# Kernel tuning notes

Hardware: AMD Instinct MI355X
Metric: run time of the kernel (lower is better)

## Reference

```python
import jax, jax.numpy as jnp
import numpy as np

EPS_NORM = 1e-12  # torch F.normalize eps
EPS_PI = 1e-8


def _l2_normalize(x, axis):
    n = jnp.sqrt(jnp.sum(x * x, axis=axis, keepdims=True))
    return x / jnp.maximum(n, EPS_NORM)


def setup_inputs() -> dict:
    key = jax.random.key(0)
    k1, _ = jax.random.split(key)
    B, L, H, E = 8, 1024, 8, 64
    queries = jax.random.normal(k1, (B, L, H, E), dtype=jnp.float32)
    temp = jnp.ones((H, 1), dtype=jnp.float32)  # nn.Parameter(torch.ones(num_heads, 1))
    return {"queries": queries, "temp": temp}


def reference(queries, temp):
    # queries: [B, L, H, E] -> w: [B, H, N, d]
    w = jnp.transpose(queries, (0, 2, 1, 3))
    # normalize over token dim (-2), square, sum over feature dim -> energy [B,H,N]
    w_normed = _l2_normalize(w, axis=-2)
    energy = jnp.sum(w_normed * w_normed, axis=-1)
    # softmax over the HEAD dim (nn.Softmax(dim=1)); temp [H,1] broadcasts over N
    Pi = jax.nn.softmax(energy * temp[None, :, :], axis=1)  # [B,H,N]
    # cosine-similarity attention matrix, mapped to [0,1]
    w_unit = _l2_normalize(w, axis=-1)
    attn_matrix = (jnp.einsum('bhnd,bhmd->bhnm', w_unit, w_unit) + 1.0) * 0.5
    # Pi normalized over tokens
    Pi_norm = Pi / (jnp.sum(Pi, axis=-1, keepdims=True) + EPS_PI)
    # dots: [B,H,1,d] = Pi_norm^T (w**2)
    dots = jnp.einsum('bhn,bhnd->bhd', Pi_norm, w * w)[:, :, None, :]
    attn = 1.0 / (1.0 + dots)  # [B,H,1,d]
    out = -(w * Pi[..., None]) * attn  # [B,H,N,d]
    out = jnp.transpose(out, (0, 2, 1, 3))  # [B,L,H,E]
    attn_reshaped = jnp.transpose(attn_matrix, (0, 2, 1, 3))  # [B,N,H,N]
    return out, attn_reshaped
```

## Files before the change

### kernel.cpp

```cpp
#include <hip/hip_runtime.h>
#include <hip/hip_bf16.h>

#define B_ 8
#define N_ 1024
#define H_ 8
#define D_ 64

typedef __attribute__((ext_vector_type(8))) short short8;
typedef __attribute__((ext_vector_type(4))) float f32x4;

__global__ __launch_bounds__(256) void k_zero(float* __restrict__ p, int n) {
    const int i = blockIdx.x * 256 + threadIdx.x;
    if (i < n) p[i] = 0.f;
}

__global__ __launch_bounds__(256) void k_colsum(const float* __restrict__ q,
                                                ushort* __restrict__ wunit,
                                                float* __restrict__ colsum) {
    const int bh = blockIdx.x, chunk = blockIdx.y;
    const int b = bh >> 3, h = bh & 7;
    const float* qb = q + (size_t)(b * N_ * H_ + h) * D_;
    __shared__ float red[16][64];
    const int t = threadIdx.x;
    const int ng = t >> 4;
    const int dq = (t & 15) * 4;
    float cx = 0.f, cy = 0.f, cz = 0.f, cw = 0.f;
    #pragma unroll
    for (int i = 0; i < 8; ++i) {
        const int n = chunk * 128 + ng + i * 16;
        const float4 v = *(const float4*)(qb + (size_t)n * (H_ * D_) + dq);
        cx += v.x * v.x; cy += v.y * v.y; cz += v.z * v.z; cw += v.w * v.w;
        float ss = v.x * v.x + v.y * v.y + v.z * v.z + v.w * v.w;
        ss += __shfl_xor(ss, 1, 16);
        ss += __shfl_xor(ss, 2, 16);
        ss += __shfl_xor(ss, 4, 16);
        ss += __shfl_xor(ss, 8, 16);
        const float invr = 1.0f / fmaxf(sqrtf(ss), 1e-12f);
        __hip_bfloat162 p0 =
            __float22bfloat162_rn(make_float2(v.x * invr, v.y * invr));
        __hip_bfloat162 p1 =
            __float22bfloat162_rn(make_float2(v.z * invr, v.w * invr));
        uint2 pk;
        pk.x = *(unsigned int*)&p0;
        pk.y = *(unsigned int*)&p1;
        *(uint2*)(wunit + ((size_t)bh * N_ + n) * D_ + dq) = pk;
    }
    red[ng][dq + 0] = cx; red[ng][dq + 1] = cy;
    red[ng][dq + 2] = cz; red[ng][dq + 3] = cw;
    __syncthreads();
    if (t < 64) {
        float s = 0.f;
        #pragma unroll
        for (int i = 0; i < 16; ++i) s += red[i][t];
        atomicAdd(&colsum[bh * 64 + t], s);
    }
}

__global__ __launch_bounds__(256) void k_energy(const float* __restrict__ q,
                                                const float* __restrict__ colsum,
                                                float* __restrict__ energy) {
    const int bh = blockIdx.x, chunk = blockIdx.y;
    const int b = bh >> 3, h = bh & 7;
    __shared__ float inv2[64];
    const int t = threadIdx.x;
    if (t < 64) inv2[t] = 1.0f / fmaxf(colsum[bh * 64 + t], 1e-24f);
    __syncthreads();
    const int n = chunk * 256 + t;
    const float4* row =
        (const float4*)(q + (size_t)(b * N_ * H_ + h) * D_ + (size_t)n * (H_ * D_));
    float e = 0.f;
    #pragma unroll
    for (int i = 0; i < 16; ++i) {
        const float4 v = row[i];
        e += v.x * v.x * inv2[4 * i + 0] + v.y * v.y * inv2[4 * i + 1] +
             v.z * v.z * inv2[4 * i + 2] + v.w * v.w * inv2[4 * i + 3];
    }
    energy[(size_t)bh * N_ + n] = e;
}

__global__ __launch_bounds__(256) void k_pi(const float* __restrict__ energy,
                                            const float* __restrict__ temp,
                                            float* __restrict__ Pi,
                                            float* __restrict__ Pisum) {
    const int idx = blockIdx.x * 256 + threadIdx.x;
    const int b = idx >> 10, n = idx & (N_ - 1);
    float e[H_];
    float m = -1e30f;
    #pragma unroll
    for (int h = 0; h < H_; ++h) {
        e[h] = energy[(size_t)(b * H_ + h) * N_ + n] * temp[h];
        m = fmaxf(m, e[h]);
    }
    float s = 0.f;
    #pragma unroll
    for (int h = 0; h < H_; ++h) { e[h] = expf(e[h] - m); s += e[h]; }
    const float inv = 1.0f / s;
    #pragma unroll
    for (int h = 0; h < H_; ++h) {
        const float p = e[h] * inv;
        Pi[(size_t)(b * H_ + h) * N_ + n] = p;
        float w = p;
        #pragma unroll
        for (int off = 32; off; off >>= 1) w += __shfl_xor(w, off, 64);
        if ((threadIdx.x & 63) == 0) atomicAdd(&Pisum[b * H_ + h], w);
    }
}

__global__ __launch_bounds__(256) void k_dots(const float* __restrict__ q,
                                              const float* __restrict__ Pi,
                                              float* __restrict__ dots) {
    const int bh = blockIdx.x, chunk = blockIdx.y;
    const int b = bh >> 3, h = bh & 7;
    const float* qb = q + (size_t)(b * N_ * H_ + h) * D_;
    const float* Pib = Pi + (size_t)bh * N_;
    __shared__ float red[16][64];
    const int t = threadIdx.x, ng = t >> 4, dq = (t & 15) * 4;
    float cx = 0.f, cy = 0.f, cz = 0.f, cw = 0.f;
    #pragma unroll
    for (int i = 0; i < 8; ++i) {
        const int n = chunk * 128 + ng + i * 16;
        const float p = Pib[n];
        const float4 v = *(const float4*)(qb + (size_t)n * (H_ * D_) + dq);
        cx += p * v.x * v.x; cy += p * v.y * v.y;
        cz += p * v.z * v.z; cw += p * v.w * v.w;
    }
    red[ng][dq + 0] = cx; red[ng][dq + 1] = cy;
    red[ng][dq + 2] = cz; red[ng][dq + 3] = cw;
    __syncthreads();
    if (t < 64) {
        float s = 0.f;
        #pragma unroll
        for (int i = 0; i < 16; ++i) s += red[i][t];
        atomicAdd(&dots[bh * 64 + t], s);
    }
}

__global__ __launch_bounds__(256) void k_attn(const float* __restrict__ dots,
                                              const float* __restrict__ Pisum,
                                              float* __restrict__ attnv) {
    const int i = blockIdx.x * 256 + threadIdx.x;
    const int bh = i >> 6;
    const float invS = 1.0f / (Pisum[bh] + 1e-8f);
    attnv[i] = 1.0f / (1.0f + dots[i] * invS);
}

__global__ __launch_bounds__(256) void k_outw(const float* __restrict__ q,
                                              const float* __restrict__ Pi,
                                              const float* __restrict__ attnv,
                                              float* __restrict__ out0) {
    const int bh = blockIdx.x, chunk = blockIdx.y;
    const int b = bh >> 3, h = bh & 7;
    __shared__ float av[64];
    const int t = threadIdx.x;
    if (t < 64) av[t] = attnv[bh * 64 + t];
    __syncthreads();
    const int n = chunk * 256 + t;
    const float p = -Pi[(size_t)bh * N_ + n];
    const float4* row =
        (const float4*)(q + (size_t)(b * N_ * H_ + h) * D_ + (size_t)n * (H_ * D_));
    float4* orow = (float4*)(out0 + ((size_t)(b * N_ + n) * H_ + h) * D_);
    #pragma unroll
    for (int i = 0; i < 16; ++i) {
        const float4 v = row[i];
        orow[i] = make_float4(v.x * p * av[4 * i + 0], v.y * p * av[4 * i + 1],
                              v.z * p * av[4 * i + 2], v.w * p * av[4 * i + 3]);
    }
}

__global__ __launch_bounds__(256) void k_gram(const ushort* __restrict__ wunit,
                                              float* __restrict__ out1) {
    const int bh = blockIdx.y;
    const int b = bh >> 3, h = bh & 7;
    const int tn = blockIdx.x & 7, tm = blockIdx.x >> 3;
    __shared__ __align__(16) char smem[36864];
    ushort(*lA)[72] = (ushort(*)[72])smem;
    ushort(*lB)[72] = (ushort(*)[72])(smem + 18432);
    float* stg = (float*)smem;
    const int t = threadIdx.x;
    const ushort* Ub = wunit + (size_t)bh * N_ * D_;

    {
        const uint4* gA = (const uint4*)(Ub + (size_t)tn * 128 * D_);
        const uint4* gB = (const uint4*)(Ub + (size_t)tm * 128 * D_);
        #pragma unroll
        for (int c = 0; c < 4; ++c) {
            const int idx = t + c * 256;
            const int row = idx >> 3, col8 = (idx & 7) * 8;
            *(uint4*)&lA[row][col8] = gA[idx];
            *(uint4*)&lB[row][col8] = gB[idx];
        }
    }
    __syncthreads();

    const int wave = t >> 6, lane = t & 63;
    const int rbase = wave * 32;
    const int arow = lane & 15;
    const int kq = (lane >> 4) * 8;

    f32x4 acc[2][8];
    #pragma unroll
    for (int i = 0; i < 2; ++i)
        #pragma unroll
        for (int j = 0; j < 8; ++j) acc[i][j] = (f32x4){0.f, 0.f, 0.f, 0.f};

    #pragma unroll
    for (int kk = 0; kk < 2; ++kk) {
        const int ko = kk * 32 + kq;
        const short8 a0 = *(const short8*)&lA[rbase + arow][ko];
        const short8 a1 = *(const short8*)&lA[rbase + 16 + arow][ko];
        #pragma unroll
        for (int tc = 0; tc < 8; ++tc) {
            const short8 bfr = *(const short8*)&lB[tc * 16 + arow][ko];
            acc[0][tc] = __builtin_amdgcn_mfma_f32_16x16x32_bf16(
                a0, bfr, acc[0][tc], 0, 0, 0);
            acc[1][tc] = __builtin_amdgcn_mfma_f32_16x16x32_bf16(
                a1, bfr, acc[1][tc], 0, 0, 0);
        }
    }
    __syncthreads();

    float* ms = stg + wave * 2112;
    const int col = lane & 15, rq = (lane >> 4) * 4;
    #pragma unroll
    for (int tr = 0; tr < 2; ++tr) {
        #pragma unroll
        for (int tc = 0; tc < 8; ++tc)
            #pragma unroll
            for (int r = 0; r < 4; ++r)
                ms[(rq + r) * 132 + tc * 16 + col] =
                    (acc[tr][tc][r] + 1.0f) * 0.5f;
        #pragma unroll
        for (int i = 0; i < 8; ++i) {
            const int f = i * 64 + lane;
            const int r2 = f >> 5, c2 = f & 31;
            const float4 v = *(const float4*)&ms[r2 * 132 + c2 * 4];
            const int n = tn * 128 + wave * 32 + tr * 16 + r2;
            const int m = tm * 128 + c2 * 4;
            *(float4*)&out1[((size_t)(b * N_ + n) * H_ + h) * N_ + m] = v;
        }
    }
}

extern "C" void kernel_launch(void* const* d_in, const int* in_sizes, int n_in,
                              void* d_out, int out_size, void* d_ws,
                              size_t ws_size, hipStream_t stream) {
    const float* q = (const float*)d_in[0];
    const float* temp = (const float*)d_in[1];
    float* out0 = (float*)d_out;
    float* out1 = out0 + (size_t)B_ * N_ * H_ * D_;

    char* ws = (char*)d_ws;
    ushort* wunit = (ushort*)ws;
    float* Pi     = (float*)(ws + 8388608);
    float* energy = (float*)(ws + 8650752);
    float* colsum = (float*)(ws + 8912896);
    float* dots   = (float*)(ws + 8929280);
    float* Pisum  = (float*)(ws + 8945664);
    float* attnv  = (float*)(ws + 8945920);

    k_zero<<<33, 256, 0, stream>>>(colsum, 8256);
    k_colsum<<<dim3(64, 8), 256, 0, stream>>>(q, wunit, colsum);
    k_energy<<<dim3(64, 4), 256, 0, stream>>>(q, colsum, energy);
    k_pi<<<32, 256, 0, stream>>>(energy, temp, Pi, Pisum);
    k_dots<<<dim3(64, 8), 256, 0, stream>>>(q, Pi, dots);
    k_attn<<<16, 256, 0, stream>>>(dots, Pisum, attnv);
    k_outw<<<dim3(64, 4), 256, 0, stream>>>(q, Pi, attnv, out0);
    k_gram<<<dim3(64, 64), 256, 0, stream>>>(wunit, out1);
}
```

Measured before the change: 334.2 us.

## Fuse reduction kernels per head and restructure Gram kernel with LDS swizzle

After: 347.1 us. +3.8%, slower.

```diff
diff --git a/kernel.cpp b/kernel.cpp
--- a/kernel.cpp
+++ b/kernel.cpp
@@ -9,25 +9,26 @@
 typedef __attribute__((ext_vector_type(8))) short short8;
 typedef __attribute__((ext_vector_type(4))) float f32x4;
 
-__global__ __launch_bounds__(256) void k_zero(float* __restrict__ p, int n) {
-    const int i = blockIdx.x * 256 + threadIdx.x;
-    if (i < n) p[i] = 0.f;
-}
-
-__global__ __launch_bounds__(256) void k_colsum(const float* __restrict__ q,
-                                                ushort* __restrict__ wunit,
-                                                float* __restrict__ colsum) {
-    const int bh = blockIdx.x, chunk = blockIdx.y;
+#define GLL(g, l)                                                         \
+    __builtin_amdgcn_global_load_lds(                                     \
+        (const __attribute__((address_space(1))) unsigned int*)(g),       \
+        (__attribute__((address_space(3))) unsigned int*)(l), 16, 0, 0)
+
+__global__ __launch_bounds__(1024) void k_prep(const float* __restrict__ q,
+                                               ushort* __restrict__ wunit,
+                                               float* __restrict__ energy) {
+    const int bh = blockIdx.x;
     const int b = bh >> 3, h = bh & 7;
     const float* qb = q + (size_t)(b * N_ * H_ + h) * D_;
-    __shared__ float red[16][64];
+    __shared__ float red[64][68];
+    __shared__ float inv2[64];
     const int t = threadIdx.x;
     const int ng = t >> 4;
     const int dq = (t & 15) * 4;
     float cx = 0.f, cy = 0.f, cz = 0.f, cw = 0.f;
     #pragma unroll
-    for (int i = 0; i < 8; ++i) {
-        const int n = chunk * 128 + ng + i * 16;
+    for (int i = 0; i < 16; ++i) {
+        const int n = i * 64 + ng;
         const float4 v = *(const float4*)(qb + (size_t)n * (H_ * D_) + dq);
         cx += v.x * v.x; cy += v.y * v.y; cz += v.z * v.z; cw += v.w * v.w;
         float ss = v.x * v.x + v.y * v.y + v.z * v.z + v.w * v.w;
@@ -45,29 +46,16 @@
         pk.y = *(unsigned int*)&p1;
         *(uint2*)(wunit + ((size_t)bh * N_ + n) * D_ + dq) = pk;
     }
-    red[ng][dq + 0] = cx; red[ng][dq + 1] = cy;
-    red[ng][dq + 2] = cz; red[ng][dq + 3] = cw;
+    *(float4*)&red[ng][dq] = make_float4(cx, cy, cz, cw);
     __syncthreads();
     if (t < 64) {
         float s = 0.f;
         #pragma unroll
-        for (int i = 0; i < 16; ++i) s += red[i][t];
-        atomicAdd(&colsum[bh * 64 + t], s);
-    }
-}
-
-__global__ __launch_bounds__(256) void k_energy(const float* __restrict__ q,
-                                                const float* __restrict__ colsum,
-                                                float* __restrict__ energy) {
-    const int bh = blockIdx.x, chunk = blockIdx.y;
-    const int b = bh >> 3, h = bh & 7;
-    __shared__ float inv2[64];
-    const int t = threadIdx.x;
-    if (t < 64) inv2[t] = 1.0f / fmaxf(colsum[bh * 64 + t], 1e-24f);
-    __syncthreads();
-    const int n = chunk * 256 + t;
-    const float4* row =
-        (const float4*)(q + (size_t)(b * N_ * H_ + h) * D_ + (size_t)n * (H_ * D_));
+        for (int i = 0; i < 64; ++i) s += red[i][t];
+        inv2[t] = 1.0f / fmaxf(s, 1e-24f);
+    }
+    __syncthreads();
+    const float4* row = (const float4*)(qb + (size_t)t * (H_ * D_));
     float e = 0.f;
     #pragma unroll
     for (int i = 0; i < 16; ++i) {
@@ -75,13 +63,12 @@
         e += v.x * v.x * inv2[4 * i + 0] + v.y * v.y * inv2[4 * i + 1] +
              v.z * v.z * inv2[4 * i + 2] + v.w * v.w * inv2[4 * i + 3];
     }
-    energy[(size_t)bh * N_ + n] = e;
+    energy[(size_t)bh * N_ + t] = e;
 }
 
 __global__ __launch_bounds__(256) void k_pi(const float* __restrict__ energy,
                                             const float* __restrict__ temp,
-                                            float* __restrict__ Pi,
-                                            float* __restrict__ Pisum) {
+                                            float* __restrict__ Pi) {
     const int idx = blockIdx.x * 256 + threadIdx.x;
     const int b = idx >> 10, n = idx & (N_ - 1);
     float e[H_];
@@ -96,148 +83,121 @@
     for (int h = 0; h < H_; ++h) { e[h] = expf(e[h] - m); s += e[h]; }
     const float inv = 1.0f / s;
     #pragma unroll
-    for (int h = 0; h < H_; ++h) {
-        const float p = e[h] * inv;
-        Pi[(size_t)(b * H_ + h) * N_ + n] = p;
-        float w = p;
-        #pragma unroll
-        for (int off = 32; off; off >>= 1) w += __shfl_xor(w, off, 64);
-        if ((threadIdx.x & 63) == 0) atomicAdd(&Pisum[b * H_ + h], w);
-    }
-}
-
-__global__ __launch_bounds__(256) void k_dots(const float* __restrict__ q,
+    for (int h = 0; h < H_; ++h)
+        Pi[(size_t)(b * H_ + h) * N_ + n] = e[h] * inv;
+}
+
+__global__ __launch_bounds__(1024) void k_out(const float* __restrict__ q,
                                               const float* __restrict__ Pi,
-                                              float* __restrict__ dots) {
-    const int bh = blockIdx.x, chunk = blockIdx.y;
+                                              float* __restrict__ out0) {
+    const int bh = blockIdx.x;
     const int b = bh >> 3, h = bh & 7;
     const float* qb = q + (size_t)(b * N_ * H_ + h) * D_;
     const float* Pib = Pi + (size_t)bh * N_;
-    __shared__ float red[16][64];
-    const int t = threadIdx.x, ng = t >> 4, dq = (t & 15) * 4;
-    float cx = 0.f, cy = 0.f, cz = 0.f, cw = 0.f;
-    #pragma unroll
-    for (int i = 0; i < 8; ++i) {
-        const int n = chunk * 128 + ng + i * 16;
+    __shared__ float red[64][68];
+    __shared__ float redP[64];
+    __shared__ float av[64];
+    __shared__ float sInv;
+    const int t = threadIdx.x;
+    const int ng = t >> 4;
+    const int dq = (t & 15) * 4;
+    float cx = 0.f, cy = 0.f, cz = 0.f, cw = 0.f, ps = 0.f;
+    #pragma unroll
+    for (int i = 0; i < 16; ++i) {
+        const int n = i * 64 + ng;
         const float p = Pib[n];
         const float4 v = *(const float4*)(qb + (size_t)n * (H_ * D_) + dq);
         cx += p * v.x * v.x; cy += p * v.y * v.y;
         cz += p * v.z * v.z; cw += p * v.w * v.w;
-    }
-    red[ng][dq + 0] = cx; red[ng][dq + 1] = cy;
-    red[ng][dq + 2] = cz; red[ng][dq + 3] = cw;
-    __syncthreads();
+        ps += p;
+    }
+    *(float4*)&red[ng][dq] = make_float4(cx, cy, cz, cw);
+    if ((t & 15) == 0) redP[ng] = ps;
+    __syncthreads();
+    float dsum = 0.f;
     if (t < 64) {
-        float s = 0.f;
-        #pragma unroll
-        for (int i = 0; i < 16; ++i) s += red[i][t];
-        atomicAdd(&dots[bh * 64 + t], s);
-    }
-}
-
-__global__ __launch_bounds__(256) void k_attn(const float* __restrict__ dots,
-                                              const float* __restrict__ Pisum,
-                                              float* __restrict__ attnv) {
-    const int i = blockIdx.x * 256 + threadIdx.x;
-    const int bh = i >> 6;
-    const float invS = 1.0f / (Pisum[bh] + 1e-8f);
-    attnv[i] = 1.0f / (1.0f + dots[i] * invS);
-}
-
-__global__ __launch_bounds__(256) void k_outw(const float* __restrict__ q,
-                                              const float* __restrict__ Pi,
-                                              const float* __restrict__ attnv,
-                                              float* __restrict__ out0) {
-    const int bh = blockIdx.x, chunk = blockIdx.y;
-    const int b = bh >> 3, h = bh & 7;
-    __shared__ float av[64];
+        #pragma unroll
+        for (int i = 0; i < 64; ++i) dsum += red[i][t];
+    }
+    if (t == 0) {
+        float S = 0.f;
+        #pragma unroll
+        for (int i = 0; i < 64; ++i) S += redP[i];
+        sInv = 1.0f / (S + 1e-8f);
+    }
+    __syncthreads();
+    if (t < 64) av[t] = 1.0f / (1.0f + dsum * sInv);
+    __syncthreads();
+    const float p = -Pib[t];
+    const float4* row = (const float4*)(qb + (size_t)t * (H_ * D_));
+    f32x4* orow = (f32x4*)(out0 + ((size_t)(b * N_ + t) * H_ + h) * D_);
+    #pragma unroll
+    for (int i = 0; i < 16; ++i) {
+        const float4 v = row[i];
+        f32x4 o = {v.x * p * av[4 * i + 0], v.y * p * av[4 * i + 1],
+                   v.z * p * av[4 * i + 2], v.w * p * av[4 * i + 3]};
+        __builtin_nontemporal_store(o, orow + i);
+    }
+}
+
+__global__ __launch_bounds__(512) void k_gram(const ushort* __restrict__ wunit,
+                                              float* __restrict__ out1) {
+    const int b = blockIdx.x;
+    const int slab = blockIdx.y;
+    __shared__ __align__(16) char smem[133120];
     const int t = threadIdx.x;
-    if (t < 64) av[t] = attnv[bh * 64 + t];
-    __syncthreads();
-    const int n = chunk * 256 + t;
-    const float p = -Pi[(size_t)bh * N_ + n];
-    const float4* row =
-        (const float4*)(q + (size_t)(b * N_ * H_ + h) * D_ + (size_t)n * (H_ * D_));
-    float4* orow = (float4*)(out0 + ((size_t)(b * N_ + n) * H_ + h) * D_);
-    #pragma unroll
-    for (int i = 0; i < 16; ++i) {
-        const float4 v = row[i];
-        orow[i] = make_float4(v.x * p * av[4 * i + 0], v.y * p * av[4 * i + 1],
-                              v.z * p * av[4 * i + 2], v.w * p * av[4 * i + 3]);
-    }
-}
-
-__global__ __launch_bounds__(256) void k_gram(const ushort* __restrict__ wunit,
-                                              float* __restrict__ out1) {
-    const int bh = blockIdx.y;
-    const int b = bh >> 3, h = bh & 7;
-    const int tn = blockIdx.x & 7, tm = blockIdx.x >> 3;
-    __shared__ __align__(16) char smem[36864];
-    ushort(*lA)[72] = (ushort(*)[72])smem;
-    ushort(*lB)[72] = (ushort(*)[72])(smem + 18432);
-    float* stg = (float*)smem;
-    const int t = threadIdx.x;
-    const ushort* Ub = wunit + (size_t)bh * N_ * D_;
-
-    {
-        const uint4* gA = (const uint4*)(Ub + (size_t)tn * 128 * D_);
-        const uint4* gB = (const uint4*)(Ub + (size_t)tm * 128 * D_);
-        #pragma unroll
-        for (int c = 0; c < 4; ++c) {
-            const int idx = t + c * 256;
-            const int row = idx >> 3, col8 = (idx & 7) * 8;
-            *(uint4*)&lA[row][col8] = gA[idx];
-            *(uint4*)&lB[row][col8] = gB[idx];
+    const int lane = t & 63, wave = t >> 6;
+    const int wm = wave >> 2, wn = wave & 3;
+    const int arow = lane & 15;
+    const int lsel = lane >> 4;
+    const int sw = arow & 7;
+    float* stgw = (float*)smem + wave * (16 * 260);
+
+    #pragma unroll 1
+    for (int h = 0; h < H_; ++h) {
+        const char* Ubh =
+            (const char*)(wunit + (size_t)(b * H_ + h) * N_ * D_);
+        #pragma unroll
+        for (int k = 0; k < 16; ++k) {
+            const int g_lin = k * 512 + t;
+            const int row = g_lin >> 3;
+            const int gsrc = (g_lin & 7) ^ (row & 7);
+            GLL(Ubh + row * 128 + gsrc * 16, smem + g_lin * 16);
         }
-    }
-    __syncthreads();
-
-    const int wave = t >> 6, lane = t & 63;
-    const int rbase = wave * 32;
-    const int arow = lane & 15;
-    const int kq = (lane >> 4) * 8;
-
-    f32x4 acc[2][8];
-    #pragma unroll
-    for (int i = 0; i < 2; ++i)
-        #pragma unroll
-        for (int j = 0; j < 8; ++j) acc[i][j] = (f32x4){0.f, 0.f, 0.f, 0.f};
-
-    #pragma unroll
-    for (int kk = 0; kk < 2; ++kk) {
-        const int ko = kk * 32 + kq;
-        const short8 a0 = *(const short8*)&lA[rbase + arow][ko];
-        const short8 a1 = *(const short8*)&lA[rbase + 16 + arow][ko];
-        #pragma unroll
-        for (int tc = 0; tc < 8; ++tc) {
-            const short8 bfr = *(const short8*)&lB[tc * 16 + arow][ko];
-            acc[0][tc] = __builtin_amdgcn_mfma_f32_16x16x32_bf16(
-                a0, bfr, acc[0][tc], 0, 0, 0);
-            acc[1][tc] = __builtin_amdgcn_mfma_f32_16x16x32_bf16(
-                a1, bfr, acc[1][tc], 0, 0, 0);
+        __syncthreads();
+        f32x4 acc[16];
+        #pragma unroll
+        for (int i = 0; i < 16; ++i) acc[i] = (f32x4){0.f, 0.f, 0.f, 0.f};
+        #pragma unroll
+        for (int kk = 0; kk < 2; ++kk) {
+            const int go = ((lsel + kk * 4) ^ sw) << 4;
+            const int rA = slab * 32 + wm * 16 + arow;
+            const short8 a = *(const short8*)(smem + rA * 128 + go);
+            #pragma unroll
+            for (int tc = 0; tc < 16; ++tc) {
+                const int rB = wn * 256 + tc * 16 + arow;
+                const short8 bv = *(const short8*)(smem + rB * 128 + go);
+                acc[tc] = __builtin_amdgcn_mfma_f32_16x16x32_bf16(
+                    a, bv, acc[tc], 0, 0, 0);
+            }
         }
-    }
-    __syncthreads();
-
-    float* ms = stg + wave * 2112;
-    const int col = lane & 15, rq = (lane >> 4) * 4;
-    #pragma unroll
-    for (int tr = 0; tr < 2; ++tr) {
-        #pragma unroll
-        for (int tc = 0; tc < 8; ++tc)
+        __syncthreads();
+        const int rq = lsel * 4;
+        #pragma unroll
+        for (int tc = 0; tc < 16; ++tc)
             #pragma unroll
             for (int r = 0; r < 4; ++r)
-                ms[(rq + r) * 132 + tc * 16 + col] =
-                    (acc[tr][tc][r] + 1.0f) * 0.5f;
-        #pragma unroll
-        for (int i = 0; i < 8; ++i) {
-            const int f = i * 64 + lane;
-            const int r2 = f >> 5, c2 = f & 31;
-            const float4 v = *(const float4*)&ms[r2 * 132 + c2 * 4];
-            const int n = tn * 128 + wave * 32 + tr * 16 + r2;
-            const int m = tm * 128 + c2 * 4;
-            *(float4*)&out1[((size_t)(b * N_ + n) * H_ + h) * N_ + m] = v;
+                stgw[(rq + r) * 260 + tc * 16 + arow] =
+                    (acc[tc][r] + 1.0f) * 0.5f;
+        #pragma unroll
+        for (int r2 = 0; r2 < 16; ++r2) {
+            const int n = slab * 32 + wm * 16 + r2;
+            const f32x4 v = *(const f32x4*)(stgw + r2 * 260 + lane * 4);
+            __builtin_nontemporal_store(
+                v, (f32x4*)(out1 + ((size_t)(b * N_ + n) * H_ + h) * N_ +
+                            wn * 256) + lane);
         }
+        __syncthreads();
     }
 }
 
@@ -253,17 +213,9 @@
     ushort* wunit = (ushort*)ws;
     float* Pi     = (float*)(ws + 8388608);
     float* energy = (float*)(ws + 8650752);
-    float* colsum = (float*)(ws + 8912896);
-    float* dots   = (float*)(ws + 8929280);
-    float* Pisum  = (float*)(ws + 8945664);
-    float* attnv  = (float*)(ws + 8945920);
-
-    k_zero<<<33, 256, 0, stream>>>(colsum, 8256);
-    k_colsum<<<dim3(64, 8), 256, 0, stream>>>(q, wunit, colsum);
-    k_energy<<<dim3(64, 4), 256, 0, stream>>>(q, colsum, energy);
-    k_pi<<<32, 256, 0, stream>>>(energy, temp, Pi, Pisum);
-    k_dots<<<dim3(64, 8), 256, 0, stream>>>(q, Pi, dots);
-    k_attn<<<16, 256, 0, stream>>>(dots, Pisum, attnv);
-    k_outw<<<dim3(64, 4), 256, 0, stream>>>(q, Pi, attnv, out0);
-    k_gram<<<dim3(64, 64), 256, 0, stream>>>(wunit, out1);
-}
+
+    k_prep<<<64, 1024, 0, stream>>>(q, wunit, energy);
+    k_pi<<<32, 256, 0, stream>>>(energy, temp, Pi);
+    k_out<<<64, 1024, 0, stream>>>(q, Pi, out0);
+    k_gram<<<dim3(8, 32), 512, 0, stream>>>(wunit, out1);
+}
```
